# Kernel tuning notes

Hardware: AMD Instinct MI355X
Metric: run time of the kernel (lower is better)

The kernel has to match this reference:

```python
import jax, jax.numpy as jnp
import numpy as np

N_NODES = 50000
N_EDGES = 600000
D_IN = 128
D_HID = 128
NUM_LAYERS = 4


def setup_inputs() -> dict:
    key = jax.random.key(0)
    ks = jax.random.split(key, 8)
    x = jax.random.normal(ks[0], (N_NODES, D_IN), dtype=jnp.float32)
    edge_index = jax.random.randint(ks[1], (2, N_EDGES), 0, N_NODES, dtype=jnp.int32)
    s = 0.05
    # first_conv: lin_rel (weight+bias) applied to aggregated neighbors, lin_root (no bias) applied to x
    W1 = jax.random.normal(ks[2], (D_IN, D_HID), dtype=jnp.float32) * s
    b1 = jnp.zeros((D_HID,), dtype=jnp.float32)
    R1 = jax.random.normal(ks[3], (D_IN, D_HID), dtype=jnp.float32) * s
    # shared conv used for layers 2..NUM_LAYERS
    W2 = jax.random.normal(ks[4], (D_HID, D_HID), dtype=jnp.float32) * s
    b2 = jnp.zeros((D_HID,), dtype=jnp.float32)
    R2 = jax.random.normal(ks[5], (D_HID, D_HID), dtype=jnp.float32) * s
    return {"x": x, "edge_index": edge_index, "W1": W1, "b1": b1, "R1": R1,
            "W2": W2, "b2": b2, "R2": R2}


def _graph_conv(x, src, dst, W, b, R, num_nodes):
    # gather source features, scatter-max into destinations (PyG GraphConv, aggr='max')
    agg = jax.ops.segment_max(x[src], dst, num_segments=num_nodes)  # [N, d]
    agg = jnp.where(jnp.isneginf(agg), 0.0, agg)  # isolated nodes -> 0 (PyG fill)
    return agg @ W + b + x @ R  # lin_rel(agg) + lin_root(x)


def reference(x, edge_index, W1, b1, R1, W2, b2, R2):
    src, dst = edge_index[0], edge_index[1]
    n = x.shape[0]
    h = jax.nn.relu(_graph_conv(x, src, dst, W1, b1, R1, n))
    for _ in range(NUM_LAYERS - 1):  # shared weights, per original module
        h = jax.nn.relu(_graph_conv(h, src, dst, W2, b2, R2, n))
    return h
```

## Files before the change

kernel.cpp:

```cpp
#include <hip/hip_runtime.h>
#include <math.h>

static constexpr int NNODES = 50000;
static constexpr int NEDGES = 600000;
static constexpr int D = 128;
static constexpr int NPART = (NNODES + 255) / 256;

typedef __attribute__((ext_vector_type(8))) short short8;
typedef __attribute__((ext_vector_type(4))) float f32x4;

static __device__ inline unsigned short f2bf_rne(float f) {
  unsigned u = __float_as_uint(f);
  unsigned r = (u + 0x7FFFu + ((u >> 16) & 1u)) >> 16;
  return (unsigned short)r;
}
static __device__ inline float bf2f(unsigned short s) {
  return __uint_as_float(((unsigned)s) << 16);
}

__global__ __launch_bounds__(256) void split_kernel(const float* __restrict__ x,
    unsigned short* __restrict__ hi, unsigned short* __restrict__ lo, int n4) {
  int i = blockIdx.x * 256 + threadIdx.x;
  if (i >= n4) return;
  f32x4 v = *(const f32x4*)(x + (size_t)i * 4);
  ushort4 h, l;
  h.x = f2bf_rne(v[0]); l.x = f2bf_rne(v[0] - bf2f(h.x));
  h.y = f2bf_rne(v[1]); l.y = f2bf_rne(v[1] - bf2f(h.y));
  h.z = f2bf_rne(v[2]); l.z = f2bf_rne(v[2] - bf2f(h.z));
  h.w = f2bf_rne(v[3]); l.w = f2bf_rne(v[3] - bf2f(h.w));
  *(ushort4*)(hi + (size_t)i * 4) = h;
  *(ushort4*)(lo + (size_t)i * 4) = l;
}


__global__ void count_kernel(const int* __restrict__ dst, int* __restrict__ cnt, int nE) {
  int i = blockIdx.x * blockDim.x + threadIdx.x;
  if (i < nE) atomicAdd(&cnt[dst[i]], 1);
}

__global__ void scan_partial(const int* __restrict__ cnt, int* __restrict__ part, int n) {
  int i = blockIdx.x * 256 + threadIdx.x;
  int v = (i < n) ? cnt[i] : 0;
#pragma unroll
  for (int off = 32; off > 0; off >>= 1) v += __shfl_down(v, off);
  __shared__ int ws[4];
  int wid = threadIdx.x >> 6, lane = threadIdx.x & 63;
  if (lane == 0) ws[wid] = v;
  __syncthreads();
  if (threadIdx.x == 0) part[blockIdx.x] = ws[0] + ws[1] + ws[2] + ws[3];
}

__global__ void scan_root(const int* __restrict__ part, int* __restrict__ pscan,
                          int* __restrict__ rs_last, int np) {
  int i = threadIdx.x;
  int v = (i < np) ? part[i] : 0;
  int incl = v;
  int lane = i & 63, wid = i >> 6;
#pragma unroll
  for (int off = 1; off < 64; off <<= 1) {
    int t = __shfl_up(incl, off);
    if (lane >= off) incl += t;
  }
  __shared__ int ws[4];
  if (lane == 63) ws[wid] = incl;
  __syncthreads();
  int woff = 0;
  for (int w = 0; w < wid; ++w) woff += ws[w];
  if (i < np) pscan[i] = woff + incl - v;
  if (i == 0) *rs_last = ws[0] + ws[1] + ws[2] + ws[3];
}

__global__ void scan_apply(const int* __restrict__ cnt, const int* __restrict__ pscan,
                           int* __restrict__ rs, int* __restrict__ cursor, int n) {
  int i = blockIdx.x * 256 + threadIdx.x;
  int v = (i < n) ? cnt[i] : 0;
  int incl = v;
  int lane = threadIdx.x & 63, wid = threadIdx.x >> 6;
#pragma unroll
  for (int off = 1; off < 64; off <<= 1) {
    int t = __shfl_up(incl, off);
    if (lane >= off) incl += t;
  }
  __shared__ int ws[4];
  if (lane == 63) ws[wid] = incl;
  __syncthreads();
  int woff = pscan[blockIdx.x];
  for (int w = 0; w < wid; ++w) woff += ws[w];
  int ex = woff + incl - v;
  if (i < n) { rs[i] = ex; cursor[i] = ex; }
}

__global__ void fill_kernel(const int* __restrict__ src, const int* __restrict__ dst,
                            int* __restrict__ cursor, int* __restrict__ csr, int nE) {
  int i = blockIdx.x * blockDim.x + threadIdx.x;
  if (i < nE) {
    int d = dst[i];
    int p = atomicAdd(&cursor[d], 1);
    csr[p] = src[i];
  }
}

struct PackArgs {
  const float* src[4];
  unsigned short* hi[4];
  unsigned short* lo[4];
};

__global__ void pack_all(PackArgs pa) {
  int mat = blockIdx.x >> 3;
  int tid = (blockIdx.x & 7) * 256 + threadIdx.x;
  const float* Wm = pa.src[mat];
  unsigned short* hi = pa.hi[mat];
  unsigned short* lo = pa.lo[mat];
  int jb = tid >> 8;
  int ks = (tid >> 6) & 3;
  int lane = tid & 63;
  int j = jb * 16 + (lane & 15);
  int k0 = ks * 32 + (lane >> 4) * 8;
#pragma unroll
  for (int e = 0; e < 8; ++e) {
    float v = Wm[(k0 + e) * D + j];
    unsigned short h = f2bf_rne(v);
    float rem = v - bf2f(h);
    unsigned short l = f2bf_rne(rem);
    hi[tid * 8 + e] = h;
    lo[tid * 8 + e] = l;
  }
}

__global__ __launch_bounds__(256) void layer_fused(
    const unsigned short* __restrict__ hhi, const unsigned short* __restrict__ hlo,
    const int* __restrict__ rs, const int* __restrict__ csr,
    const unsigned short* __restrict__ Whi, const unsigned short* __restrict__ Wlo,
    const unsigned short* __restrict__ Rhi, const unsigned short* __restrict__ Rlo,
    const float* __restrict__ bias, float* __restrict__ outf,
    unsigned short* __restrict__ ohi, unsigned short* __restrict__ olo, int nrows) {
  __shared__ unsigned lds[4][1024];
  const int lane = threadIdx.x & 63;
  const int wv = threadIdx.x >> 6;
  const int m_lo = lane & 15;
  const int sub = lane >> 4;
  const int r_base = blockIdx.x * 64 + wv * 16;
  const unsigned* __restrict__ xb = (const unsigned*)hhi;
  const float NEG = __uint_as_float(0xFF800000u);
  unsigned* ldsw = &lds[wv][0];

  for (int i = 0; i < 16; ++i) {
    int row = r_base + i;
    int beg = 0, end = 0;
    if (row < nrows) { beg = rs[row]; end = rs[row + 1]; }
    float ax = NEG, ay = NEG;
    int j = beg;
    for (; j + 8 <= end; j += 8) {
      int s[8];
#pragma unroll
      for (int u = 0; u < 8; ++u) s[u] = csr[j + u];
      unsigned v[8];
#pragma unroll
      for (int u = 0; u < 8; ++u) v[u] = xb[(size_t)s[u] * 64 + lane];
#pragma unroll
      for (int u = 0; u < 8; ++u) {
        ax = fmaxf(ax, __uint_as_float(v[u] << 16));
        ay = fmaxf(ay, __uint_as_float(v[u] & 0xFFFF0000u));
      }
    }
    for (; j < end; ++j) {
      unsigned v = xb[(size_t)csr[j] * 64 + lane];
      ax = fmaxf(ax, __uint_as_float(v << 16));
      ay = fmaxf(ay, __uint_as_float(v & 0xFFFF0000u));
    }
    if (beg == end) { ax = 0.f; ay = 0.f; }
    unsigned p = (__float_as_uint(ax) >> 16) | (__float_as_uint(ay) & 0xFFFF0000u);
    ldsw[(i * 256 + ((lane * 4) ^ ((i & 7) << 4))) >> 2] = p;
  }
  __syncthreads();

  f32x4 acc[8];
#pragma unroll
  for (int jb = 0; jb < 8; ++jb) acc[jb] = (f32x4)0.f;

  float bv[8];
#pragma unroll
  for (int jb = 0; jb < 8; ++jb) bv[jb] = bias[jb * 16 + m_lo];

  const char* ldsc = (const char*)&lds[wv][0];
  for (int ks = 0; ks < 4; ++ks) {
    short8 fa, fhh, fhl;
    {
      int ri = m_lo;
      int bofs = ri * 256 + (((ks * 64) + (sub * 16)) ^ ((ri & 7) << 4));
      fa = *(const short8*)(ldsc + bofs);
      int row = r_base + m_lo; if (row >= nrows) row = nrows - 1;
      const size_t ro = (size_t)row * D + ks * 32 + sub * 8;
      fhh = *(const short8*)(hhi + ro);
      fhl = *(const short8*)(hlo + ro);
    }
#pragma unroll
    for (int jb = 0; jb < 8; ++jb) {
      const int pidx = ((jb * 4 + ks) * 64 + lane) * 8;
      short8 bwhi = *(const short8*)(Whi + pidx);
      short8 bwlo = *(const short8*)(Wlo + pidx);
      short8 brhi = *(const short8*)(Rhi + pidx);
      short8 brlo = *(const short8*)(Rlo + pidx);
      acc[jb] = __builtin_amdgcn_mfma_f32_16x16x32_bf16(fa,  bwhi, acc[jb], 0, 0, 0);
      acc[jb] = __builtin_amdgcn_mfma_f32_16x16x32_bf16(fa,  bwlo, acc[jb], 0, 0, 0);
      acc[jb] = __builtin_amdgcn_mfma_f32_16x16x32_bf16(fhh, brhi, acc[jb], 0, 0, 0);
      acc[jb] = __builtin_amdgcn_mfma_f32_16x16x32_bf16(fhl, brhi, acc[jb], 0, 0, 0);
      acc[jb] = __builtin_amdgcn_mfma_f32_16x16x32_bf16(fhh, brlo, acc[jb], 0, 0, 0);
    }
  }

#pragma unroll
  for (int jb = 0; jb < 8; ++jb) {
#pragma unroll
    for (int r = 0; r < 4; ++r) {
      int row = r_base + sub * 4 + r;
      if (row < nrows) {
        float v = fmaxf(acc[jb][r] + bv[jb], 0.f);
        size_t o = (size_t)row * D + jb * 16 + m_lo;
        if (outf) {
          outf[o] = v;
        } else {
          unsigned short h = f2bf_rne(v);
          ohi[o] = h;
          olo[o] = f2bf_rne(v - bf2f(h));
        }
      }
    }
  }
}


extern "C" void kernel_launch(void* const* d_in, const int* in_sizes, int n_in,
                              void* d_out, int out_size, void* d_ws, size_t ws_size,
                              hipStream_t stream) {
  const float* x  = (const float*)d_in[0];
  const int*   ei = (const int*)d_in[1];
  const float* W1 = (const float*)d_in[2];
  const float* b1 = (const float*)d_in[3];
  const float* R1 = (const float*)d_in[4];
  const float* W2 = (const float*)d_in[5];
  const float* b2 = (const float*)d_in[6];
  const float* R2 = (const float*)d_in[7];
  float* out = (float*)d_out;

  const int* src = ei;
  const int* dst = ei + NEDGES;

  char* ws = (char*)d_ws;
  size_t off = 0;
  auto alloc = [&](size_t bytes) -> void* {
    off = (off + 511) & ~(size_t)511;
    void* p = ws + off;
    off += bytes;
    return p;
  };
  const size_t NF = (size_t)NNODES * D;
  unsigned short* xhi  = (unsigned short*)alloc(sizeof(short) * NF);
  unsigned short* xlo  = (unsigned short*)alloc(sizeof(short) * NF);
  unsigned short* hAhi = (unsigned short*)alloc(sizeof(short) * NF);
  unsigned short* hAlo = (unsigned short*)alloc(sizeof(short) * NF);
  unsigned short* hBhi = (unsigned short*)alloc(sizeof(short) * NF);
  unsigned short* hBlo = (unsigned short*)alloc(sizeof(short) * NF);
  int* cnt    = (int*)alloc(sizeof(int) * NNODES);
  int* rs     = (int*)alloc(sizeof(int) * (NNODES + 1));
  int* cursor = (int*)alloc(sizeof(int) * NNODES);
  int* csr    = (int*)alloc(sizeof(int) * NEDGES);
  int* part   = (int*)alloc(sizeof(int) * NPART);
  int* pscan  = (int*)alloc(sizeof(int) * NPART);
  const int PACKN = 2048 * 8;
  unsigned short* w1hi = (unsigned short*)alloc(sizeof(short) * PACKN);
  unsigned short* w1lo = (unsigned short*)alloc(sizeof(short) * PACKN);
  unsigned short* r1hi = (unsigned short*)alloc(sizeof(short) * PACKN);
  unsigned short* r1lo = (unsigned short*)alloc(sizeof(short) * PACKN);
  unsigned short* w2hi = (unsigned short*)alloc(sizeof(short) * PACKN);
  unsigned short* w2lo = (unsigned short*)alloc(sizeof(short) * PACKN);
  unsigned short* r2hi = (unsigned short*)alloc(sizeof(short) * PACKN);
  unsigned short* r2lo = (unsigned short*)alloc(sizeof(short) * PACKN);

  split_kernel<<<(int)(NF / 4 + 255) / 256, 256, 0, stream>>>(x, xhi, xlo, (int)(NF / 4));

  PackArgs pa;
  pa.src[0] = W1; pa.hi[0] = w1hi; pa.lo[0] = w1lo;
  pa.src[1] = R1; pa.hi[1] = r1hi; pa.lo[1] = r1lo;
  pa.src[2] = W2; pa.hi[2] = w2hi; pa.lo[2] = w2lo;
  pa.src[3] = R2; pa.hi[3] = r2hi; pa.lo[3] = r2lo;
  pack_all<<<32, 256, 0, stream>>>(pa);

  hipMemsetAsync(cnt, 0, sizeof(int) * NNODES, stream);
  count_kernel<<<(NEDGES + 255) / 256, 256, 0, stream>>>(dst, cnt, NEDGES);
  scan_partial<<<NPART, 256, 0, stream>>>(cnt, part, NNODES);
  scan_root<<<1, 256, 0, stream>>>(part, pscan, &rs[NNODES], NPART);
  scan_apply<<<NPART, 256, 0, stream>>>(cnt, pscan, rs, cursor, NNODES);
  fill_kernel<<<(NEDGES + 255) / 256, 256, 0, stream>>>(src, dst, cursor, csr, NEDGES);

  const int grid = (NNODES + 63) / 64;

  auto layer = [&](const unsigned short* hhi, const unsigned short* hlo,
                   const unsigned short* whi, const unsigned short* wlo,
                   const unsigned short* rhi, const unsigned short* rlo,
                   const float* b, float* outf, unsigned short* ohi, unsigned short* olo) {
    layer_fused<<<grid, 256, 0, stream>>>(hhi, hlo, rs, csr, whi, wlo, rhi, rlo,
                                          b, outf, ohi, olo, NNODES);
  };

  layer(xhi,  xlo,  w1hi, w1lo, r1hi, r1lo, b1, nullptr, hAhi, hAlo);
  layer(hAhi, hAlo, w2hi, w2lo, r2hi, r2lo, b2, nullptr, hBhi, hBlo);
  layer(hBhi, hBlo, w2hi, w2lo, r2hi, r2lo, b2, nullptr, hAhi, hAlo);
  layer(hAhi, hAlo, w2hi, w2lo, r2hi, r2lo, b2, out, nullptr, nullptr);
}
```

Before: 473.2 us.

## Balance edge aggregation across waves with LDS atomic max over block tile

Replaces the per-row, per-wave gather loop with an edge-balanced scheme. Each block's edge range is split evenly among its four waves, and partial maxima are written into a 64x128 fp32 LDS tile using order-preserving integer atomicMax. A new csr_row array records the destination of every edge. The aim is to remove load imbalance from variable node degree, but it adds many LDS atomics, a 32KB LDS tile that can lower occupancy, and extra setup and finalize passes.

New measurement: 571.0 us. +20.7%, slower.

```diff
diff --git a/kernel.cpp b/kernel.cpp
--- a/kernel.cpp
+++ b/kernel.cpp
@@ -16,6 +16,12 @@
 }
 static __device__ inline float bf2f(unsigned short s) {
   return __uint_as_float(((unsigned)s) << 16);
+}
+static __device__ inline unsigned map_ord(unsigned u) {
+  return (u & 0x80000000u) ? ~u : (u | 0x80000000u);
+}
+static __device__ inline unsigned unmap_ord(unsigned m) {
+  return (m & 0x80000000u) ? (m ^ 0x80000000u) : ~m;
 }
 
 __global__ __launch_bounds__(256) void split_kernel(const float* __restrict__ x,
@@ -91,12 +97,14 @@
 }
 
 __global__ void fill_kernel(const int* __restrict__ src, const int* __restrict__ dst,
-                            int* __restrict__ cursor, int* __restrict__ csr, int nE) {
+                            int* __restrict__ cursor, int* __restrict__ csr,
+                            int* __restrict__ csr_row, int nE) {
   int i = blockIdx.x * blockDim.x + threadIdx.x;
   if (i < nE) {
     int d = dst[i];
     int p = atomicAdd(&cursor[d], 1);
     csr[p] = src[i];
+    csr_row[p] = d;
   }
 }
 
@@ -131,50 +139,78 @@
 __global__ __launch_bounds__(256) void layer_fused(
     const unsigned short* __restrict__ hhi, const unsigned short* __restrict__ hlo,
     const int* __restrict__ rs, const int* __restrict__ csr,
+    const int* __restrict__ csr_row,
     const unsigned short* __restrict__ Whi, const unsigned short* __restrict__ Wlo,
     const unsigned short* __restrict__ Rhi, const unsigned short* __restrict__ Rlo,
     const float* __restrict__ bias, float* __restrict__ outf,
     unsigned short* __restrict__ ohi, unsigned short* __restrict__ olo, int nrows) {
-  __shared__ unsigned lds[4][1024];
-  const int lane = threadIdx.x & 63;
-  const int wv = threadIdx.x >> 6;
+  __shared__ unsigned tile[64 * 128];
+  const int tid = threadIdx.x;
+  const int lane = tid & 63;
+  const int wv = tid >> 6;
   const int m_lo = lane & 15;
   const int sub = lane >> 4;
-  const int r_base = blockIdx.x * 64 + wv * 16;
+  const int base = blockIdx.x * 64;
   const unsigned* __restrict__ xb = (const unsigned*)hhi;
-  const float NEG = __uint_as_float(0xFF800000u);
-  unsigned* ldsw = &lds[wv][0];
-
-  for (int i = 0; i < 16; ++i) {
-    int row = r_base + i;
-    int beg = 0, end = 0;
-    if (row < nrows) { beg = rs[row]; end = rs[row + 1]; }
-    float ax = NEG, ay = NEG;
-    int j = beg;
-    for (; j + 8 <= end; j += 8) {
-      int s[8];
-#pragma unroll
-      for (int u = 0; u < 8; ++u) s[u] = csr[j + u];
-      unsigned v[8];
-#pragma unroll
-      for (int u = 0; u < 8; ++u) v[u] = xb[(size_t)s[u] * 64 + lane];
-#pragma unroll
-      for (int u = 0; u < 8; ++u) {
-        ax = fmaxf(ax, __uint_as_float(v[u] << 16));
-        ay = fmaxf(ay, __uint_as_float(v[u] & 0xFFFF0000u));
+
+  {
+    const unsigned MINF = 0x007FFFFFu;
+    uint4 m4 = make_uint4(MINF, MINF, MINF, MINF);
+#pragma unroll
+    for (int i = 0; i < 8; ++i)
+      *(uint4*)&tile[tid * 4 + i * 1024] = m4;
+  }
+  __syncthreads();
+
+  const int erows = (base + 64 < nrows) ? base + 64 : nrows;
+  const int eb = rs[base];
+  const int ee = rs[erows];
+  const int total = ee - eb;
+  const int per = (total + 3) >> 2;
+  int my_beg = eb + wv * per;
+  int my_end = my_beg + per; if (my_end > ee) my_end = ee;
+  for (int g = my_beg; g < my_end; g += 64) {
+    const int navail = (my_end - g < 64) ? my_end - g : 64;
+    int sv = 0, rv = 0;
+    if (lane < navail) { sv = csr[g + lane]; rv = csr_row[g + lane] - base; }
+    for (int e = 0; e < navail; ++e) {
+      int s = __shfl(sv, e);
+      int rr = __shfl(rv, e);
+      unsigned v = xb[(size_t)s * 64 + lane];
+      unsigned m0 = map_ord(v << 16);
+      unsigned m1 = map_ord(v & 0xFFFF0000u);
+      atomicMax(&tile[rr * 128 + 2 * lane], m0);
+      atomicMax(&tile[rr * 128 + 2 * lane + 1], m1);
+    }
+  }
+  __syncthreads();
+
+  {
+    const int lr = tid >> 2, fq = tid & 3;
+    unsigned mv[32];
+#pragma unroll
+    for (int f = 0; f < 32; ++f) mv[f] = tile[lr * 128 + fq * 32 + f];
+    const int grow = base + lr;
+    bool zero = true;
+    if (grow < nrows) zero = (rs[grow] == rs[grow + 1]);
+    __syncthreads();
+#pragma unroll
+    for (int gq = 0; gq < 4; ++gq) {
+      uint4 w;
+      unsigned pk[4];
+#pragma unroll
+      for (int k = 0; k < 4; ++k) {
+        unsigned uA = unmap_ord(mv[gq * 8 + 2 * k]);
+        unsigned uB = unmap_ord(mv[gq * 8 + 2 * k + 1]);
+        pk[k] = zero ? 0u : ((uA >> 16) | (uB & 0xFFFF0000u));
       }
-    }
-    for (; j < end; ++j) {
-      unsigned v = xb[(size_t)csr[j] * 64 + lane];
-      ax = fmaxf(ax, __uint_as_float(v << 16));
-      ay = fmaxf(ay, __uint_as_float(v & 0xFFFF0000u));
-    }
-    if (beg == end) { ax = 0.f; ay = 0.f; }
-    unsigned p = (__float_as_uint(ax) >> 16) | (__float_as_uint(ay) & 0xFFFF0000u);
-    ldsw[(i * 256 + ((lane * 4) ^ ((i & 7) << 4))) >> 2] = p;
-  }
-  __syncthreads();
-
+      w.x = pk[0]; w.y = pk[1]; w.z = pk[2]; w.w = pk[3];
+      *(uint4*)((char*)tile + lr * 512 + ((fq * 64 + gq * 16) ^ ((lr & 7) << 4))) = w;
+    }
+  }
+  __syncthreads();
+
+  const int r_base = base + wv * 16;
   f32x4 acc[8];
 #pragma unroll
   for (int jb = 0; jb < 8; ++jb) acc[jb] = (f32x4)0.f;
@@ -183,12 +219,12 @@
 #pragma unroll
   for (int jb = 0; jb < 8; ++jb) bv[jb] = bias[jb * 16 + m_lo];
 
-  const char* ldsc = (const char*)&lds[wv][0];
+  const char* ldsc = (const char*)tile;
+  const int ri = wv * 16 + m_lo;
   for (int ks = 0; ks < 4; ++ks) {
     short8 fa, fhh, fhl;
     {
-      int ri = m_lo;
-      int bofs = ri * 256 + (((ks * 64) + (sub * 16)) ^ ((ri & 7) << 4));
+      int bofs = ri * 512 + (((ks * 64) + (sub * 16)) ^ ((ri & 7) << 4));
       fa = *(const short8*)(ldsc + bofs);
       int row = r_base + m_lo; if (row >= nrows) row = nrows - 1;
       const size_t ro = (size_t)row * D + ks * 32 + sub * 8;
@@ -262,12 +298,13 @@
   unsigned short* hAlo = (unsigned short*)alloc(sizeof(short) * NF);
   unsigned short* hBhi = (unsigned short*)alloc(sizeof(short) * NF);
   unsigned short* hBlo = (unsigned short*)alloc(sizeof(short) * NF);
-  int* cnt    = (int*)alloc(sizeof(int) * NNODES);
-  int* rs     = (int*)alloc(sizeof(int) * (NNODES + 1));
-  int* cursor = (int*)alloc(sizeof(int) * NNODES);
-  int* csr    = (int*)alloc(sizeof(int) * NEDGES);
-  int* part   = (int*)alloc(sizeof(int) * NPART);
-  int* pscan  = (int*)alloc(sizeof(int) * NPART);
+  int* cnt     = (int*)alloc(sizeof(int) * NNODES);
+  int* rs      = (int*)alloc(sizeof(int) * (NNODES + 1));
+  int* cursor  = (int*)alloc(sizeof(int) * NNODES);
+  int* csr     = (int*)alloc(sizeof(int) * NEDGES);
+  int* csr_row = (int*)alloc(sizeof(int) * NEDGES);
+  int* part    = (int*)alloc(sizeof(int) * NPART);
+  int* pscan   = (int*)alloc(sizeof(int) * NPART);
   const int PACKN = 2048 * 8;
   unsigned short* w1hi = (unsigned short*)alloc(sizeof(short) * PACKN);
   unsigned short* w1lo = (unsigned short*)alloc(sizeof(short) * PACKN);
@@ -292,7 +329,7 @@
   scan_partial<<<NPART, 256, 0, stream>>>(cnt, part, NNODES);
   scan_root<<<1, 256, 0, stream>>>(part, pscan, &rs[NNODES], NPART);
   scan_apply<<<NPART, 256, 0, stream>>>(cnt, pscan, rs, cursor, NNODES);
-  fill_kernel<<<(NEDGES + 255) / 256, 256, 0, stream>>>(src, dst, cursor, csr, NEDGES);
+  fill_kernel<<<(NEDGES + 255) / 256, 256, 0, stream>>>(src, dst, cursor, csr, csr_row, NEDGES);
 
   const int grid = (NNODES + 63) / 64;
 
@@ -300,7 +337,7 @@
                    const unsigned short* whi, const unsigned short* wlo,
                    const unsigned short* rhi, const unsigned short* rlo,
                    const float* b, float* outf, unsigned short* ohi, unsigned short* olo) {
-    layer_fused<<<grid, 256, 0, stream>>>(hhi, hlo, rs, csr, whi, wlo, rhi, rlo,
+    layer_fused<<<grid, 256, 0, stream>>>(hhi, hlo, rs, csr, csr_row, whi, wlo, rhi, rlo,
                                           b, outf, ohi, olo, NNODES);
   };
 
```
